# Kernel tuning notes

Hardware: AMD Instinct MI355X
Metric: run time of the kernel (lower is better)

## Reference

```python
import jax, jax.numpy as jnp
from jax import lax
import numpy as np

PAD = 3
COEFF_POS = jnp.array([-2.0, 15.0, -60.0, 20.0, 30.0, -3.0]) / 60.0
COEFF_NEG = jnp.array([3.0, -30.0, -20.0, 60.0, -15.0, 2.0]) / 60.0
EPI_TOL = 1e-5
N_TERMS = 19  # k = 1..19 as in the torch loop


def geo_cyclic_pad(x, p=PAD):
    # Cyclic in longitude; across the poles: flip latitude and shift lon by 180 deg.
    W = x.shape[-1]
    top = jnp.flip(jnp.roll(x[:, :, :p, :], W // 2, axis=-1), axis=2)
    bot = jnp.flip(jnp.roll(x[:, :, -p:, :], W // 2, axis=-1), axis=2)
    x = jnp.concatenate([top, x, bot], axis=2)
    return jnp.concatenate([x[..., -p:], x, x[..., :p]], axis=-1)


def _corr6(x, k, axis):
    # cross-correlation with a length-6 kernel along `axis` (== F.conv2d with 1x6/6x1 kernel)
    n = x.shape[axis] - 5
    out = k[0] * lax.slice_in_dim(x, 0, n, axis=axis)
    for j in range(1, 6):
        out = out + k[j] * lax.slice_in_dim(x, j, j + n, axis=axis)
    return out


def upwind_derivative(q_padded, velocity, dx, axis):
    # 5th-order upwind finite difference with sign-dependent stencil selection
    H, W = velocity.shape[2], velocity.shape[3]
    cp = COEFF_POS.astype(q_padded.dtype)
    cn = COEFF_NEG.astype(q_padded.dtype)
    d_pos = _corr6(q_padded, cp, axis)
    d_neg = _corr6(q_padded, cn, axis)
    if axis == 3:  # longitude
        d_pos = d_pos[:, :, PAD:-PAD, :W]
        d_neg = d_neg[:, :, PAD:-PAD, 1:W + 1]
    else:  # latitude (axis == 2)
        d_pos = d_pos[:, :, :H, PAD:-PAD]
        d_neg = d_neg[:, :, 1:H + 1, PAD:-PAD]
    return jnp.where(velocity > 0, d_pos, d_neg) / dx


def compute_rhs(q, u, v, dlat, dlon):
    qp = geo_cyclic_pad(q)
    dq_dlon = upwind_derivative(qp, u, dlon, axis=3)
    dq_dlat = upwind_derivative(qp, v, dlat, axis=2)
    return -u * dq_dlon - v * dq_dlat


def phi1_times_vector(dt, rhs_fn, vector):
    # phi_1(dt*J) v = v + sum_{k>=1} (dt J)^k / (k+1)! v ; early break when term max-norm < tol
    def step(carry, k):
        term, result, done = carry
        new_term = rhs_fn(term) * (dt / (k + 1.0))
        small = jnp.max(jnp.abs(new_term)) < EPI_TOL
        term = jnp.where(done, term, new_term)
        result = jnp.where(done | small, result, result + new_term)
        return (term, result, done | small), None
    ks = jnp.arange(1, N_TERMS + 1, dtype=vector.dtype)
    (_, result, _), _ = lax.scan(step, (vector, vector, jnp.array(False)), ks)
    return result


def setup_inputs() -> dict:
    key = jax.random.key(0)
    ks = jax.random.split(key, 9)
    B, hidden_dim, num_vels = 1, 256, 16
    H, W = 181, 360  # ERA5 1-degree grid
    hidden_features = jax.random.normal(ks[0], (B, hidden_dim, H, W), jnp.float32)
    u = jax.random.normal(ks[1], (B, num_vels, H, W), jnp.float32)
    v = jax.random.normal(ks[2], (B, num_vels, H, W), jnp.float32)
    lat = jnp.linspace(-jnp.pi / 2, jnp.pi / 2, H)
    lon = jnp.linspace(0.0, 2.0 * jnp.pi, W, endpoint=False)
    dlat = (lat[1] - lat[0]).astype(jnp.float32)
    dlon = (lon[1] - lon[0]).astype(jnp.float32)
    dt = jnp.float32(1e-3)  # small enough that the Taylor series converges below EPI_TOL
    W_down = jax.random.normal(ks[3], (num_vels, hidden_dim), jnp.float32) * (1.0 / np.sqrt(hidden_dim))
    b_down = jax.random.normal(ks[4], (num_vels,), jnp.float32) * 0.01
    dw = jax.random.normal(ks[5], (num_vels,), jnp.float32)
    db = jax.random.normal(ks[6], (num_vels,), jnp.float32) * 0.01
    W_up = jax.random.normal(ks[7], (hidden_dim, num_vels), jnp.float32) * (1.0 / np.sqrt(num_vels))
    b_up = jax.random.normal(ks[8], (hidden_dim,), jnp.float32) * 0.01
    return {"hidden_features": hidden_features, "u": u, "v": v, "dt": dt,
            "dlat": dlat, "dlon": dlon, "W_down": W_down, "b_down": b_down,
            "dw": dw, "db": db, "W_up": W_up, "b_up": b_up}


def reference(hidden_features, u, v, dt, dlat, dlon, W_down, b_down, dw, db, W_up, b_up):
    # down projection (CLinear == 1x1 conv)
    q = jnp.einsum('oc,bchw->bohw', W_down, hidden_features) + b_down[None, :, None, None]
    F_n = compute_rhs(q, u, v, dlat, dlon)
    rhs_fn = lambda vec: compute_rhs(vec, u, v, dlat, dlon)  # Jacobian action (rhs is linear in q)
    phi1_F = phi1_times_vector(dt, rhs_fn, F_n)
    updated = q + phi1_F * dt
    # up projection (SepConv k=1 == depthwise 1x1 then pointwise 1x1)
    dwc = updated * dw[None, :, None, None] + db[None, :, None, None]
    return jnp.einsum('oc,bchw->bohw', W_up, dwc) + b_up[None, :, None, None]
```

## Files before the change

### kernel.cpp

```cpp
#include <hip/hip_runtime.h>
#include <hip/hip_fp16.h>

#define HH 181
#define WW 360
#define NPIX (HH*WW)
#define NCH 16
#define NHID 256
#define NPIX16 (NCH*NPIX)
#define NG4 (NPIX16/4)
#define NPG4 (NPIX/4)
#define GPR (WW/4)
#define GPC (NPIX/4)
#define NPASS 6

typedef __attribute__((ext_vector_type(8))) short bf16x8;
typedef __attribute__((ext_vector_type(4))) float f32x4;

__device__ __forceinline__ unsigned short f2bf(float x) {
    union { float f; unsigned u; } c; c.f = x;
    unsigned r = c.u + 0x7FFFu + ((c.u >> 16) & 1u);
    return (unsigned short)(r >> 16);
}

__device__ __forceinline__ void h4tof(const void* p, float* f) {
    uint2 t = *(const uint2*)p;
    union { unsigned w; __half2 h; } a, b;
    a.w = t.x; b.w = t.y;
    float2 f01 = __half22float2(a.h), f23 = __half22float2(b.h);
    f[0] = f01.x; f[1] = f01.y; f[2] = f23.x; f[3] = f23.y;
}

__device__ __forceinline__ void f4toh(void* p, float a, float b, float c, float d) {
    union { __half2 h; unsigned w; } x, y;
    x.h = __floats2half2_rn(a, b);
    y.h = __floats2half2_rn(c, d);
    *(uint2*)p = make_uint2(x.w, y.w);
}

__global__ __launch_bounds__(128) void down_kernel(
        const float* __restrict__ hid,
        const float* __restrict__ Wd,
        const float* __restrict__ b_down,
        const float* __restrict__ u,
        const float* __restrict__ v,
        const float* __restrict__ dlon_p,
        const float* __restrict__ dlat_p,
        float* __restrict__ q,
        unsigned* __restrict__ uvh) {
    const int lid = threadIdx.x & 63, wid = threadIdx.x >> 6;
    const int c16 = lid & 15;
    const int g   = lid >> 4;
    const int pix0 = blockIdx.x * 128 + wid * 64;
    const int pbase = min(pix0 + 4 * c16, NPIX - 4);

    bf16x8 a[8];
#pragma unroll
    for (int kk = 0; kk < 8; ++kk) {
        const float* wp = Wd + c16 * NHID + kk * 32 + g * 8;
        float4 w0 = *(const float4*)wp;
        float4 w1 = *(const float4*)(wp + 4);
        bf16x8 t;
        t[0] = (short)f2bf(w0.x); t[1] = (short)f2bf(w0.y);
        t[2] = (short)f2bf(w0.z); t[3] = (short)f2bf(w0.w);
        t[4] = (short)f2bf(w1.x); t[5] = (short)f2bf(w1.y);
        t[6] = (short)f2bf(w1.z); t[7] = (short)f2bf(w1.w);
        a[kk] = t;
    }

    f32x4 acc[4];
#pragma unroll
    for (int t = 0; t < 4; ++t)
#pragma unroll
        for (int r = 0; r < 4; ++r) acc[t][r] = b_down[g * 4 + r];

#pragma unroll
    for (int kk = 0; kk < 8; ++kk) {
        float4 F[8];
#pragma unroll
        for (int j = 0; j < 8; ++j)
            F[j] = *(const float4*)(hid + (size_t)(kk * 32 + g * 8 + j) * NPIX + pbase);
        bf16x8 b0, b1, b2, b3;
#pragma unroll
        for (int j = 0; j < 8; ++j) {
            b0[j] = (short)f2bf(F[j].x);
            b1[j] = (short)f2bf(F[j].y);
            b2[j] = (short)f2bf(F[j].z);
            b3[j] = (short)f2bf(F[j].w);
        }
        acc[0] = __builtin_amdgcn_mfma_f32_16x16x32_bf16(a[kk], b0, acc[0], 0, 0, 0);
        acc[1] = __builtin_amdgcn_mfma_f32_16x16x32_bf16(a[kk], b1, acc[1], 0, 0, 0);
        acc[2] = __builtin_amdgcn_mfma_f32_16x16x32_bf16(a[kk], b2, acc[2], 0, 0, 0);
        acc[3] = __builtin_amdgcn_mfma_f32_16x16x32_bf16(a[kk], b3, acc[3], 0, 0, 0);
    }

#pragma unroll
    for (int t = 0; t < 4; ++t) {
        const int px = pix0 + 4 * c16 + t;
        if (px < NPIX) {
#pragma unroll
            for (int r = 0; r < 4; ++r)
                q[(g * 4 + r) * NPIX + px] = acc[t][r];
        }
    }

    const float il = 1.0f / dlon_p[0], ia = 1.0f / dlat_p[0];
    const int px0b = blockIdx.x * 128;
#pragma unroll
    for (int it = 0; it < 16; ++it) {
        int idx = it * 128 + threadIdx.x;
        int ch  = idx >> 7;
        int px  = px0b + (idx & 127);
        if (px < NPIX) {
            int gidx = ch * NPIX + px;
            union { __half2 h; unsigned w; } cv;
            cv.h = __floats2half2_rn(u[gidx] * il, v[gidx] * ia);
            uvh[gidx] = cv.w;
        }
    }
}

__global__ __launch_bounds__(256) void pass_kernel(
        const float* __restrict__ qin,
        const unsigned* __restrict__ tin,
        unsigned* __restrict__ tout,
        const unsigned* __restrict__ uvh,
        unsigned* __restrict__ result,
        const float* __restrict__ dt_p,
        int k) {
    const float cp0 = -2.0f/60.0f, cp1 = 15.0f/60.0f, cp2 = -60.0f/60.0f,
                cp3 = 20.0f/60.0f, cp4 = 30.0f/60.0f, cp5 = -3.0f/60.0f;
    const float cn0 =  3.0f/60.0f, cn1 = -30.0f/60.0f, cn2 = -20.0f/60.0f,
                cn3 = 60.0f/60.0f, cn4 = -15.0f/60.0f, cn5 =  2.0f/60.0f;

    const int g4 = blockIdx.x * 256 + threadIdx.x;
    if (g4 >= NG4) return;
    const float scale = (k == 0) ? 1.0f : dt_p[0] / (float)(k + 1);

    const int ch  = g4 / GPC;
    const int rem = g4 - ch * GPC;
    const int h   = rem / GPR;
    const int bi  = rem - h * GPR;
    const int w0  = bi * 4;
    const int wf0 = (w0 >= WW / 2) ? (w0 - WW / 2) : (w0 + WW / 2);

    float Wn[12];
    float S[7][4];
    if (k == 0) {
        const float* base = qin + ch * NPIX;
        const float4* rowv = (const float4*)(base + h * WW);
        float4 Af = rowv[bi == 0 ? GPR - 1 : bi - 1];
        float4 Bf = rowv[bi];
        float4 Cf = rowv[bi == GPR - 1 ? 0 : bi + 1];
        Wn[0]=Af.x; Wn[1]=Af.y; Wn[2]=Af.z; Wn[3]=Af.w;
        Wn[4]=Bf.x; Wn[5]=Bf.y; Wn[6]=Bf.z; Wn[7]=Bf.w;
        Wn[8]=Cf.x; Wn[9]=Cf.y; Wn[10]=Cf.z; Wn[11]=Cf.w;
#pragma unroll
        for (int d = 0; d < 7; ++d) {
            int rr = h + d - 3, cb = w0;
            if (rr < 0)           { rr = -1 - rr;        cb = wf0; }
            else if (rr > HH - 1) { rr = 2*HH - 1 - rr;  cb = wf0; }
            float4 t = *(const float4*)(base + rr * WW + cb);
            S[d][0]=t.x; S[d][1]=t.y; S[d][2]=t.z; S[d][3]=t.w;
        }
    } else {
        const __half* base = (const __half*)tin + (size_t)ch * NPIX;
        const __half* row = base + h * WW;
        h4tof(row + (bi == 0 ? GPR - 1 : bi - 1) * 4, Wn);
        h4tof(row + bi * 4, Wn + 4);
        h4tof(row + (bi == GPR - 1 ? 0 : bi + 1) * 4, Wn + 8);
#pragma unroll
        for (int d = 0; d < 7; ++d) {
            int rr = h + d - 3, cb = w0;
            if (rr < 0)           { rr = -1 - rr;        cb = wf0; }
            else if (rr > HH - 1) { rr = 2*HH - 1 - rr;  cb = wf0; }
            h4tof(base + rr * WW + cb, S[d]);
        }
    }

    const int gi = ch * NPIX + h * WW + w0;
    const uint4 P = *(const uint4*)(uvh + gi);
    const unsigned Pw[4] = {P.x, P.y, P.z, P.w};

    float o4[4];
#pragma unroll
    for (int j = 0; j < 4; ++j) {
        float dpl = cp0*Wn[j+1] + cp1*Wn[j+2] + cp2*Wn[j+3]
                  + cp3*Wn[j+4] + cp4*Wn[j+5] + cp5*Wn[j+6];
        float dnl = cn0*Wn[j+2] + cn1*Wn[j+3] + cn2*Wn[j+4]
                  + cn3*Wn[j+5] + cn4*Wn[j+6] + cn5*Wn[j+7];
        float dpa = cp0*S[0][j] + cp1*S[1][j] + cp2*S[2][j]
                  + cp3*S[3][j] + cp4*S[4][j] + cp5*S[5][j];
        float dna = cn0*S[1][j] + cn1*S[2][j] + cn2*S[3][j]
                  + cn3*S[4][j] + cn4*S[5][j] + cn5*S[6][j];
        union { unsigned w; __half2 h; } cv; cv.w = Pw[j];
        float uu = __low2float(cv.h);
        float vv = __high2float(cv.h);
        o4[j] = (-uu * (uu > 0.0f ? dpl : dnl)
                 -vv * (vv > 0.0f ? dpa : dna)) * scale;
    }

    if (k < NPASS - 1)
        f4toh((__half*)tout + gi, o4[0], o4[1], o4[2], o4[3]);

    __half* rp = (__half*)result + gi;
    if (k == 0) {
        f4toh(rp, o4[0], o4[1], o4[2], o4[3]);
    } else if (k == NPASS - 1) {
        float r4[4]; h4tof(rp, r4);
        f4toh(rp, r4[0]+o4[0], r4[1]+o4[1], r4[2]+o4[2], r4[3]+o4[3]);
    } else if ((k & 1) == 0) {
        float r4[4]; h4tof(rp, r4);
        f4toh(rp, r4[0]+Wn[4]+o4[0], r4[1]+Wn[5]+o4[1],
                  r4[2]+Wn[6]+o4[2], r4[3]+Wn[7]+o4[3]);
    }
}

__global__ __launch_bounds__(256) void up_kernel(const float* __restrict__ q,
                                                 const unsigned* __restrict__ result,
                                                 const float* __restrict__ dt_p,
                                                 const float* __restrict__ dw,
                                                 const float* __restrict__ db,
                                                 const float* __restrict__ Wu,
                                                 const float* __restrict__ b_up,
                                                 float* __restrict__ out) {
    const int g = blockIdx.x * 256 + threadIdx.x;
    if (g >= NPG4) return;
    const int pix0 = g * 4;
    const int c0 = blockIdx.y * 32;
    const float dt = dt_p[0];

    float d[NCH][4];
#pragma unroll
    for (int o = 0; o < NCH; ++o) {
        const int gb = o * NPIX + pix0;
        float4 Q = *(const float4*)(q + gb);
        float r4[4]; h4tof((const __half*)result + gb, r4);
        float dwo = dw[o], dbo = db[o];
        d[o][0] = (Q.x + r4[0] * dt) * dwo + dbo;
        d[o][1] = (Q.y + r4[1] * dt) * dwo + dbo;
        d[o][2] = (Q.z + r4[2] * dt) * dwo + dbo;
        d[o][3] = (Q.w + r4[3] * dt) * dwo + dbo;
    }
#pragma unroll 4
    for (int cc = 0; cc < 32; ++cc) {
        const int c = c0 + cc;
        const float bc = b_up[c];
        float a0 = bc, a1 = bc, a2 = bc, a3 = bc;
#pragma unroll
        for (int o = 0; o < NCH; ++o) {
            float wv = Wu[c * NCH + o];
            a0 += wv * d[o][0]; a1 += wv * d[o][1];
            a2 += wv * d[o][2]; a3 += wv * d[o][3];
        }
        *(float4*)(out + c * NPIX + pix0) = make_float4(a0, a1, a2, a3);
    }
}

extern "C" void kernel_launch(void* const* d_in, const int* in_sizes, int n_in,
                              void* d_out, int out_size, void* d_ws, size_t ws_size,
                              hipStream_t stream) {
    const float* hidden = (const float*)d_in[0];
    const float* u      = (const float*)d_in[1];
    const float* v      = (const float*)d_in[2];
    const float* dt_p   = (const float*)d_in[3];
    const float* dlat_p = (const float*)d_in[4];
    const float* dlon_p = (const float*)d_in[5];
    const float* W_down = (const float*)d_in[6];
    const float* b_down = (const float*)d_in[7];
    const float* dw     = (const float*)d_in[8];
    const float* db     = (const float*)d_in[9];
    const float* W_up   = (const float*)d_in[10];
    const float* b_up   = (const float*)d_in[11];
    float* out = (float*)d_out;

    float* ws = (float*)d_ws;
    float* q          = ws;
    unsigned* result  = (unsigned*)(ws + (size_t)NPIX16);
    unsigned* t0      = (unsigned*)(ws + (size_t)NPIX16 + NPIX16/2);
    unsigned* t1      = (unsigned*)(ws + (size_t)2 * NPIX16);
    unsigned* uvh     = (unsigned*)out;

    const int nbg = (NG4 + 255) / 256;
    const int nbu = (NPG4 + 255) / 256;
    const int nbd = (NPIX + 127) / 128;

    down_kernel<<<nbd, 128, 0, stream>>>(hidden, W_down, b_down, u, v,
                                         dlon_p, dlat_p, q, uvh);

    pass_kernel<<<nbg, 256, 0, stream>>>(q, t1, t0, uvh, result, dt_p, 0);
    for (int k = 1; k < NPASS; ++k) {
        unsigned* tin  = (k & 1) ? t0 : t1;
        unsigned* tout = (k & 1) ? t1 : t0;
        pass_kernel<<<nbg, 256, 0, stream>>>(q, tin, tout, uvh, result, dt_p, k);
    }

    up_kernel<<<dim3(nbu, 8), 256, 0, stream>>>(q, result, dt_p, dw, db,
                                                W_up, b_up, out);
}
```

Baseline: 77.29 us.

## Fuse pairs of stencil passes via LDS row bands with halo recompute

Replaces the six separate stencil-pass launches with two fused kernels plus a final pass. Each fused kernel processes a 4-row band per channel: it computes the first pass for the band plus a 3-row halo into shared memory, then computes the second pass from shared memory. This removes intermediate global round trips and kernel launches, at the cost of recomputing halo rows and giving each block a serial loop with a barrier between its two stages.

```diff
diff --git a/kernel.cpp b/kernel.cpp
--- a/kernel.cpp
+++ b/kernel.cpp
@@ -11,7 +11,8 @@
 #define NPG4 (NPIX/4)
 #define GPR (WW/4)
 #define GPC (NPIX/4)
-#define NPASS 6
+#define BR 4
+#define NBANDS 46
 
 typedef __attribute__((ext_vector_type(8))) short bf16x8;
 typedef __attribute__((ext_vector_type(4))) float f32x4;
@@ -35,6 +36,66 @@
     x.h = __floats2half2_rn(a, b);
     y.h = __floats2half2_rn(c, d);
     *(uint2*)p = make_uint2(x.w, y.w);
+}
+
+__device__ __forceinline__ void upwind4(const float Wn[12], const float S[7][4],
+                                        const unsigned Pw[4], float scale,
+                                        float o4[4]) {
+    const float cp0 = -2.0f/60.0f, cp1 = 15.0f/60.0f, cp2 = -60.0f/60.0f,
+                cp3 = 20.0f/60.0f, cp4 = 30.0f/60.0f, cp5 = -3.0f/60.0f;
+    const float cn0 =  3.0f/60.0f, cn1 = -30.0f/60.0f, cn2 = -20.0f/60.0f,
+                cn3 = 60.0f/60.0f, cn4 = -15.0f/60.0f, cn5 =  2.0f/60.0f;
+#pragma unroll
+    for (int j = 0; j < 4; ++j) {
+        float dpl = cp0*Wn[j+1] + cp1*Wn[j+2] + cp2*Wn[j+3]
+                  + cp3*Wn[j+4] + cp4*Wn[j+5] + cp5*Wn[j+6];
+        float dnl = cn0*Wn[j+2] + cn1*Wn[j+3] + cn2*Wn[j+4]
+                  + cn3*Wn[j+5] + cn4*Wn[j+6] + cn5*Wn[j+7];
+        float dpa = cp0*S[0][j] + cp1*S[1][j] + cp2*S[2][j]
+                  + cp3*S[3][j] + cp4*S[4][j] + cp5*S[5][j];
+        float dna = cn0*S[1][j] + cn1*S[2][j] + cn2*S[3][j]
+                  + cn3*S[4][j] + cn4*S[5][j] + cn5*S[6][j];
+        union { unsigned w; __half2 h; } cv; cv.w = Pw[j];
+        float uu = __low2float(cv.h);
+        float vv = __high2float(cv.h);
+        o4[j] = (-uu * (uu > 0.0f ? dpl : dnl)
+                 -vv * (vv > 0.0f ? dpa : dna)) * scale;
+    }
+}
+
+__device__ __forceinline__ void taps_global(const float* qb, const __half* tb,
+                                            int first, int h, int bi, int wf0,
+                                            float Wn[12], float S[7][4]) {
+    const int w0 = bi * 4;
+    if (first) {
+        const float4* rowv = (const float4*)(qb + h * WW);
+        float4 Af = rowv[bi == 0 ? GPR - 1 : bi - 1];
+        float4 Bf = rowv[bi];
+        float4 Cf = rowv[bi == GPR - 1 ? 0 : bi + 1];
+        Wn[0]=Af.x; Wn[1]=Af.y; Wn[2]=Af.z; Wn[3]=Af.w;
+        Wn[4]=Bf.x; Wn[5]=Bf.y; Wn[6]=Bf.z; Wn[7]=Bf.w;
+        Wn[8]=Cf.x; Wn[9]=Cf.y; Wn[10]=Cf.z; Wn[11]=Cf.w;
+#pragma unroll
+        for (int d = 0; d < 7; ++d) {
+            int rr = h + d - 3, cb = w0;
+            if (rr < 0)           { rr = -1 - rr;        cb = wf0; }
+            else if (rr > HH - 1) { rr = 2*HH - 1 - rr;  cb = wf0; }
+            float4 t = *(const float4*)(qb + rr * WW + cb);
+            S[d][0]=t.x; S[d][1]=t.y; S[d][2]=t.z; S[d][3]=t.w;
+        }
+    } else {
+        const __half* row = tb + h * WW;
+        h4tof(row + (bi == 0 ? GPR - 1 : bi - 1) * 4, Wn);
+        h4tof(row + bi * 4, Wn + 4);
+        h4tof(row + (bi == GPR - 1 ? 0 : bi + 1) * 4, Wn + 8);
+#pragma unroll
+        for (int d = 0; d < 7; ++d) {
+            int rr = h + d - 3, cb = w0;
+            if (rr < 0)           { rr = -1 - rr;        cb = wf0; }
+            else if (rr > HH - 1) { rr = 2*HH - 1 - rr;  cb = wf0; }
+            h4tof(tb + rr * WW + cb, S[d]);
+        }
+    }
 }
 
 __global__ __launch_bounds__(128) void down_kernel(
@@ -119,100 +180,106 @@
     }
 }
 
-__global__ __launch_bounds__(256) void pass_kernel(
+__global__ __launch_bounds__(256) void fused2_kernel(
         const float* __restrict__ qin,
         const unsigned* __restrict__ tin,
-        unsigned* __restrict__ tout,
+        unsigned* __restrict__ toutB,
         const unsigned* __restrict__ uvh,
         unsigned* __restrict__ result,
         const float* __restrict__ dt_p,
-        int k) {
-    const float cp0 = -2.0f/60.0f, cp1 = 15.0f/60.0f, cp2 = -60.0f/60.0f,
-                cp3 = 20.0f/60.0f, cp4 = 30.0f/60.0f, cp5 = -3.0f/60.0f;
-    const float cn0 =  3.0f/60.0f, cn1 = -30.0f/60.0f, cn2 = -20.0f/60.0f,
-                cn3 = 60.0f/60.0f, cn4 = -15.0f/60.0f, cn5 =  2.0f/60.0f;
-
-    const int g4 = blockIdx.x * 256 + threadIdx.x;
+        int ka) {
+    __shared__ __half tA[10 * WW];
+    const int ch   = blockIdx.x / NBANDS;
+    const int band = blockIdx.x - ch * NBANDS;
+    const int r0   = band * BR;
+    const int vr   = min(BR, HH - r0);
+    const int lo   = max(0, r0 - 3);
+    const int hi   = min(HH - 1, r0 + vr - 1 + 3);
+    const int rowsA = hi - lo + 1;
+    const int tid  = threadIdx.x;
+    const float dt = dt_p[0];
+    const float scaleA = (ka == 0) ? 1.0f : dt / (float)(ka + 1);
+    const float scaleB = dt / (float)(ka + 2);
+    const int first = (ka == 0);
+
+    const float*  qb = qin + ch * NPIX;
+    const __half* tb = (const __half*)tin + (size_t)ch * NPIX;
+    const unsigned* uvb = uvh + ch * NPIX;
+
+    for (int i = tid; i < rowsA * GPR; i += 256) {
+        const int hh = lo + i / GPR;
+        const int bi = i - (i / GPR) * GPR;
+        const int w0 = bi * 4;
+        const int wf0 = (w0 >= WW / 2) ? (w0 - WW / 2) : (w0 + WW / 2);
+        float Wn[12], S[7][4];
+        taps_global(qb, tb, first, hh, bi, wf0, Wn, S);
+        const uint4 P = *(const uint4*)(uvb + hh * WW + w0);
+        const unsigned Pw[4] = {P.x, P.y, P.z, P.w};
+        float o4[4];
+        upwind4(Wn, S, Pw, scaleA, o4);
+        f4toh(&tA[(hh - lo) * WW + w0], o4[0], o4[1], o4[2], o4[3]);
+    }
+    __syncthreads();
+
+    for (int i = tid; i < vr * GPR; i += 256) {
+        const int h  = r0 + i / GPR;
+        const int bi = i - (i / GPR) * GPR;
+        const int w0 = bi * 4;
+        const int wf0 = (w0 >= WW / 2) ? (w0 - WW / 2) : (w0 + WW / 2);
+        float Wn[12], S[7][4];
+        const __half* lrow = &tA[(h - lo) * WW];
+        h4tof(lrow + (bi == 0 ? GPR - 1 : bi - 1) * 4, Wn);
+        h4tof(lrow + bi * 4, Wn + 4);
+        h4tof(lrow + (bi == GPR - 1 ? 0 : bi + 1) * 4, Wn + 8);
+#pragma unroll
+        for (int d = 0; d < 7; ++d) {
+            int rr = h + d - 3, cb = w0;
+            if (rr < 0)           { rr = -1 - rr;        cb = wf0; }
+            else if (rr > HH - 1) { rr = 2*HH - 1 - rr;  cb = wf0; }
+            h4tof(&tA[(rr - lo) * WW + cb], S[d]);
+        }
+        const int gi = ch * NPIX + h * WW + w0;
+        const uint4 P = *(const uint4*)(uvh + gi);
+        const unsigned Pw[4] = {P.x, P.y, P.z, P.w};
+        float o4[4];
+        upwind4(Wn, S, Pw, scaleB, o4);
+        f4toh((__half*)toutB + gi, o4[0], o4[1], o4[2], o4[3]);
+        __half* rp = (__half*)result + gi;
+        if (ka == 0) {
+            f4toh(rp, Wn[4]+o4[0], Wn[5]+o4[1], Wn[6]+o4[2], Wn[7]+o4[3]);
+        } else {
+            float r4[4]; h4tof(rp, r4);
+            f4toh(rp, r4[0]+Wn[4]+o4[0], r4[1]+Wn[5]+o4[1],
+                      r4[2]+Wn[6]+o4[2], r4[3]+Wn[7]+o4[3]);
+        }
+    }
+}
+
+__global__ __launch_bounds__(128) void last_kernel(
+        const unsigned* __restrict__ tin,
+        const unsigned* __restrict__ uvh,
+        unsigned* __restrict__ result,
+        const float* __restrict__ dt_p) {
+    const int g4 = blockIdx.x * 128 + threadIdx.x;
     if (g4 >= NG4) return;
-    const float scale = (k == 0) ? 1.0f : dt_p[0] / (float)(k + 1);
-
+    const float scale = dt_p[0] / 5.0f;
     const int ch  = g4 / GPC;
     const int rem = g4 - ch * GPC;
     const int h   = rem / GPR;
     const int bi  = rem - h * GPR;
     const int w0  = bi * 4;
     const int wf0 = (w0 >= WW / 2) ? (w0 - WW / 2) : (w0 + WW / 2);
-
-    float Wn[12];
-    float S[7][4];
-    if (k == 0) {
-        const float* base = qin + ch * NPIX;
-        const float4* rowv = (const float4*)(base + h * WW);
-        float4 Af = rowv[bi == 0 ? GPR - 1 : bi - 1];
-        float4 Bf = rowv[bi];
-        float4 Cf = rowv[bi == GPR - 1 ? 0 : bi + 1];
-        Wn[0]=Af.x; Wn[1]=Af.y; Wn[2]=Af.z; Wn[3]=Af.w;
-        Wn[4]=Bf.x; Wn[5]=Bf.y; Wn[6]=Bf.z; Wn[7]=Bf.w;
-        Wn[8]=Cf.x; Wn[9]=Cf.y; Wn[10]=Cf.z; Wn[11]=Cf.w;
-#pragma unroll
-        for (int d = 0; d < 7; ++d) {
-            int rr = h + d - 3, cb = w0;
-            if (rr < 0)           { rr = -1 - rr;        cb = wf0; }
-            else if (rr > HH - 1) { rr = 2*HH - 1 - rr;  cb = wf0; }
-            float4 t = *(const float4*)(base + rr * WW + cb);
-            S[d][0]=t.x; S[d][1]=t.y; S[d][2]=t.z; S[d][3]=t.w;
-        }
-    } else {
-        const __half* base = (const __half*)tin + (size_t)ch * NPIX;
-        const __half* row = base + h * WW;
-        h4tof(row + (bi == 0 ? GPR - 1 : bi - 1) * 4, Wn);
-        h4tof(row + bi * 4, Wn + 4);
-        h4tof(row + (bi == GPR - 1 ? 0 : bi + 1) * 4, Wn + 8);
-#pragma unroll
-        for (int d = 0; d < 7; ++d) {
-            int rr = h + d - 3, cb = w0;
-            if (rr < 0)           { rr = -1 - rr;        cb = wf0; }
-            else if (rr > HH - 1) { rr = 2*HH - 1 - rr;  cb = wf0; }
-            h4tof(base + rr * WW + cb, S[d]);
-        }
-    }
-
+    float Wn[12], S[7][4];
+    taps_global(nullptr, (const __half*)tin + (size_t)ch * NPIX, 0,
+                h, bi, wf0, Wn, S);
     const int gi = ch * NPIX + h * WW + w0;
     const uint4 P = *(const uint4*)(uvh + gi);
     const unsigned Pw[4] = {P.x, P.y, P.z, P.w};
-
     float o4[4];
-#pragma unroll
-    for (int j = 0; j < 4; ++j) {
-        float dpl = cp0*Wn[j+1] + cp1*Wn[j+2] + cp2*Wn[j+3]
-                  + cp3*Wn[j+4] + cp4*Wn[j+5] + cp5*Wn[j+6];
-        float dnl = cn0*Wn[j+2] + cn1*Wn[j+3] + cn2*Wn[j+4]
-                  + cn3*Wn[j+5] + cn4*Wn[j+6] + cn5*Wn[j+7];
-        float dpa = cp0*S[0][j] + cp1*S[1][j] + cp2*S[2][j]
-                  + cp3*S[3][j] + cp4*S[4][j] + cp5*S[5][j];
-        float dna = cn0*S[1][j] + cn1*S[2][j] + cn2*S[3][j]
-                  + cn3*S[4][j] + cn4*S[5][j] + cn5*S[6][j];
-        union { unsigned w; __half2 h; } cv; cv.w = Pw[j];
-        float uu = __low2float(cv.h);
-        float vv = __high2float(cv.h);
-        o4[j] = (-uu * (uu > 0.0f ? dpl : dnl)
-                 -vv * (vv > 0.0f ? dpa : dna)) * scale;
-    }
-
-    if (k < NPASS - 1)
-        f4toh((__half*)tout + gi, o4[0], o4[1], o4[2], o4[3]);
-
+    upwind4(Wn, S, Pw, scale, o4);
     __half* rp = (__half*)result + gi;
-    if (k == 0) {
-        f4toh(rp, o4[0], o4[1], o4[2], o4[3]);
-    } else if (k == NPASS - 1) {
-        float r4[4]; h4tof(rp, r4);
-        f4toh(rp, r4[0]+o4[0], r4[1]+o4[1], r4[2]+o4[2], r4[3]+o4[3]);
-    } else if ((k & 1) == 0) {
-        float r4[4]; h4tof(rp, r4);
-        f4toh(rp, r4[0]+Wn[4]+o4[0], r4[1]+Wn[5]+o4[1],
-                  r4[2]+Wn[6]+o4[2], r4[3]+Wn[7]+o4[3]);
-    }
+    float r4[4]; h4tof(rp, r4);
+    f4toh(rp, r4[0]+o4[0], r4[1]+o4[1], r4[2]+o4[2], r4[3]+o4[3]);
 }
 
 __global__ __launch_bounds__(256) void up_kernel(const float* __restrict__ q,
@@ -276,24 +343,20 @@
     float* ws = (float*)d_ws;
     float* q          = ws;
     unsigned* result  = (unsigned*)(ws + (size_t)NPIX16);
-    unsigned* t0      = (unsigned*)(ws + (size_t)NPIX16 + NPIX16/2);
-    unsigned* t1      = (unsigned*)(ws + (size_t)2 * NPIX16);
+    unsigned* t1      = (unsigned*)(ws + (size_t)NPIX16 + NPIX16/2);
+    unsigned* t3      = (unsigned*)(ws + (size_t)2 * NPIX16);
     unsigned* uvh     = (unsigned*)out;
 
-    const int nbg = (NG4 + 255) / 256;
+    const int nbf = NCH * NBANDS;
+    const int nbl = (NG4 + 127) / 128;
     const int nbu = (NPG4 + 255) / 256;
     const int nbd = (NPIX + 127) / 128;
 
     down_kernel<<<nbd, 128, 0, stream>>>(hidden, W_down, b_down, u, v,
                                          dlon_p, dlat_p, q, uvh);
-
-    pass_kernel<<<nbg, 256, 0, stream>>>(q, t1, t0, uvh, result, dt_p, 0);
-    for (int k = 1; k < NPASS; ++k) {
-        unsigned* tin  = (k & 1) ? t0 : t1;
-        unsigned* tout = (k & 1) ? t1 : t0;
-        pass_kernel<<<nbg, 256, 0, stream>>>(q, tin, tout, uvh, result, dt_p, k);
-    }
-
+    fused2_kernel<<<nbf, 256, 0, stream>>>(q, nullptr, t1, uvh, result, dt_p, 0);
+    fused2_kernel<<<nbf, 256, 0, stream>>>(nullptr, t1, t3, uvh, result, dt_p, 2);
+    last_kernel<<<nbl, 128, 0, stream>>>(t3, uvh, result, dt_p);
     up_kernel<<<dim3(nbu, 8), 256, 0, stream>>>(q, result, dt_p, dw, db,
                                                 W_up, b_up, out);
 }
```

Result: no change. 75.80 us (-1.9%).
